# Performance work log

Hardware: AMD Instinct MI355X
Metric: run time of the kernel (lower is better)

## Reference

```python
import jax, jax.numpy as jnp
import numpy as np

# Dims: batch, seq, model dim, heads, routes-per-query, bleed-over alpha
B, S, D, H, K_ROUTES = 4, 512, 1024, 16, 64
HD = D // H                      # head_dim = 64
SCALE = 1.0 / float(np.sqrt(HD))
ALPHA = 0.25                     # neighbor bleed-over (forward arg default 0.0; >0 here)
CAUSAL = True
NEG = jnp.float32(-1e9)


def _build_routes(seq_len: int, k: int, depth: int = 8) -> np.ndarray:
    """Cantor-coordinate based positional routes (mirrors _build_positional_routes)."""
    pos = np.arange(seq_len, dtype=np.float64)
    x = pos / max(1, seq_len - 1)
    x = np.clip(x, 1e-6, 1.0 - 1e-6)
    val = np.zeros_like(x)
    factor = 0.5
    for _ in range(depth):
        xs = x * 3.0
        digit = xs.astype(np.int64)
        frac = xs - digit
        val = val + (digit == 2).astype(np.float64) * factor
        x = frac
        factor *= 0.5
    coords = np.clip(val, 0.0, 1.0)
    dist = np.abs(coords[:, None] - coords[None, :])            # [S,S]
    routes = np.argsort(dist, axis=1, kind='stable')[:, :k]     # k smallest distances
    return routes.astype(np.int32)


def setup_inputs() -> dict:
    key = jax.random.key(0)
    k0, k1, k2 = jax.random.split(key, 3)
    x = jax.random.normal(k0, (B, S, D), dtype=jnp.float32)
    # nn.Linear weights stored pre-transposed as [in, out] for clean matmul
    w_qkv = jax.random.normal(k1, (D, 3 * D), dtype=jnp.float32) * (1.0 / np.sqrt(D))
    b_qkv = jnp.zeros((3 * D,), dtype=jnp.float32)
    w_out = jax.random.normal(k2, (D, D), dtype=jnp.float32) * (1.0 / np.sqrt(D))
    b_out = jnp.zeros((D,), dtype=jnp.float32)
    routes = jnp.asarray(_build_routes(S, K_ROUTES), dtype=jnp.int32)  # [S, K]
    return {"x": x, "w_qkv": w_qkv, "b_qkv": b_qkv,
            "w_out": w_out, "b_out": b_out, "routes": routes}


def reference(x, w_qkv, b_qkv, w_out, b_out, routes):
    # QKV projection: [B,S,3D] -> [3,B,H,S,hd]
    qkv = (x @ w_qkv + b_qkv).reshape(B, S, 3, H, HD).transpose(2, 0, 3, 1, 4)
    q, k, v = qkv[0], qkv[1], qkv[2]                 # each [B,H,S,hd]

    r = routes                                        # [S,K]
    k_g = jnp.take(k, r, axis=2)                      # [B,H,S,K,hd]
    v_g = jnp.take(v, r, axis=2)
    if ALPHA > 0.0:
        rl = jnp.clip(r - 1, 0, S - 1)
        rr = jnp.clip(r + 1, 0, S - 1)
        k_g = (1.0 - ALPHA) * k_g + (ALPHA / 2.0) * (jnp.take(k, rl, axis=2) + jnp.take(k, rr, axis=2))
        v_g = (1.0 - ALPHA) * v_g + (ALPHA / 2.0) * (jnp.take(v, rl, axis=2) + jnp.take(v, rr, axis=2))

    scores = jnp.einsum('bhqd,bhqkd->bhqk', q, k_g) * SCALE   # [B,H,S,K]
    if CAUSAL:
        # route index > query position is masked (each query always routes to itself)
        mask = r > jnp.arange(S, dtype=r.dtype)[:, None]       # [S,K]
        scores = jnp.where(mask[None, None], NEG, scores)

    attn = jax.nn.softmax(scores, axis=-1)
    out = jnp.einsum('bhqk,bhqkd->bhqd', attn, v_g)            # [B,H,S,hd]
    out = out.transpose(0, 2, 1, 3).reshape(B, S, D)
    return out @ w_out + b_out
```

## Files before the change

### kernel.cpp

```cpp
#include <hip/hip_runtime.h>
#include <hip/hip_bf16.h>

#define BB 4
#define SS 512
#define DD 1024
#define HH 16
#define KR 64
#define HDIM 64
#define THREE_D 3072
#define M_ROWS 2048
#define SCALE_F 0.125f

typedef __attribute__((ext_vector_type(8))) short short8;
typedef __attribute__((ext_vector_type(4))) float floatx4;

union F8 { short8 s; unsigned int u[4]; unsigned short h[8]; };

__device__ inline unsigned short f2bf(float f){
    union{float f; unsigned int u;} c; c.f = f;
    unsigned int u = c.u;
    return (unsigned short)((u + 0x7fffu + ((u >> 16) & 1u)) >> 16);
}

#define GLOAD_LDS16(g, l)                                                     \
    __builtin_amdgcn_global_load_lds(                                         \
        (const __attribute__((address_space(1))) unsigned int*)(g),           \
        (__attribute__((address_space(3))) unsigned int*)(l), 16, 0, 0)

__global__ __launch_bounds__(256) void cvtA_kernel(const float* __restrict__ x,
                                                   unsigned short* __restrict__ out)
{
    int gid = blockIdx.x * 256 + threadIdx.x;
    int r  = gid & 127;
    int c  = (gid >> 7) & 3;
    int kt = (gid >> 9) & 31;
    int mt = gid >> 14;
    const float* src = x + ((size_t)(mt * 128 + r)) * 1024 + kt * 32 + c * 8;
    float4 a = *(const float4*)src;
    float4 b = *(const float4*)(src + 4);
    F8 o;
    o.h[0] = f2bf(a.x); o.h[1] = f2bf(a.y); o.h[2] = f2bf(a.z); o.h[3] = f2bf(a.w);
    o.h[4] = f2bf(b.x); o.h[5] = f2bf(b.y); o.h[6] = f2bf(b.z); o.h[7] = f2bf(b.w);
    *(uint4*)(out + (size_t)gid * 8) = *(uint4*)&o;
}

__global__ __launch_bounds__(256) void cvtB_kernel(const float* __restrict__ w,
                                                   unsigned short* __restrict__ out, int N)
{
    int gid = blockIdx.x * 256 + threadIdx.x;
    int r  = gid & 127;
    int c  = (gid >> 7) & 3;
    int kt = (gid >> 9) & 31;
    int nt = gid >> 14;
    int n = nt * 128 + r;
    int kbase = kt * 32 + c * 8;
    F8 o;
#pragma unroll
    for (int j = 0; j < 8; ++j)
        o.h[j] = f2bf(w[(size_t)(kbase + j) * N + n]);
    *(uint4*)(out + (size_t)gid * 8) = *(uint4*)&o;
}

template<int EPI>
__global__ __launch_bounds__(256) void gemm_mfma(
    const unsigned short* __restrict__ Asw,
    const unsigned short* __restrict__ Bsw,
    const float* __restrict__ bias,
    float* __restrict__ Cout,
    unsigned short* __restrict__ qb, float* __restrict__ k_ws, float* __restrict__ v_ws,
    int N)
{
    __shared__ __align__(16) unsigned short Alds[4096];
    __shared__ __align__(16) unsigned short Blds[4096];

    const int tid  = threadIdx.x;
    const int lane = tid & 63;
    const int wid  = tid >> 6;
    const int l15  = lane & 15;
    const int quad = lane >> 4;
    const int wm   = (wid >> 1) * 64;
    const int wn   = (wid & 1) * 64;

    const unsigned short* Ak = Asw + (size_t)blockIdx.y * 131072;
    const unsigned short* Bk = Bsw + (size_t)blockIdx.x * 131072;

    floatx4 acc[4][4];
#pragma unroll
    for (int i = 0; i < 4; ++i)
#pragma unroll
        for (int j = 0; j < 4; ++j) acc[i][j] = (floatx4){0.f, 0.f, 0.f, 0.f};

    for (int kt = 0; kt < 32; ++kt) {
        const unsigned short* ga = Ak + kt * 4096 + wid * 1024 + lane * 8;
        const unsigned short* gb = Bk + kt * 4096 + wid * 1024 + lane * 8;
        GLOAD_LDS16(ga,       Alds + wid * 1024);
        GLOAD_LDS16(ga + 512, Alds + wid * 1024 + 512);
        GLOAD_LDS16(gb,       Blds + wid * 1024);
        GLOAD_LDS16(gb + 512, Blds + wid * 1024 + 512);
        __syncthreads();

        F8 af[4], bf[4];
#pragma unroll
        for (int mi = 0; mi < 4; ++mi)
            af[mi] = *(const F8*)(Alds + (size_t)(quad * 128 + wm + mi * 16 + l15) * 8);
#pragma unroll
        for (int ni = 0; ni < 4; ++ni)
            bf[ni] = *(const F8*)(Blds + (size_t)(quad * 128 + wn + ni * 16 + l15) * 8);
#pragma unroll
        for (int mi = 0; mi < 4; ++mi)
#pragma unroll
            for (int ni = 0; ni < 4; ++ni)
                acc[mi][ni] = __builtin_amdgcn_mfma_f32_16x16x32_bf16(
                    af[mi].s, bf[ni].s, acc[mi][ni], 0, 0, 0);
        __syncthreads();
    }

    const int m0 = blockIdx.y * 128;
    const int n0 = blockIdx.x * 128;
#pragma unroll
    for (int mi = 0; mi < 4; ++mi) {
#pragma unroll
        for (int ni = 0; ni < 4; ++ni) {
            int col = n0 + wn + ni * 16 + l15;
            float bv = bias[col];
#pragma unroll
            for (int r = 0; r < 4; ++r) {
                int row = m0 + wm + mi * 16 + quad * 4 + r;
                float val = acc[mi][ni][r] + bv;
                if (EPI == 0) {
                    Cout[(size_t)row * N + col] = val;
                } else {
                    int which = col >> 10, rem = col & 1023;
                    int h = rem >> 6, hd = rem & 63;
                    int b = row >> 9, s = row & 511;
                    size_t off = (((size_t)(b * HH + h) * SS) + s) * HDIM + hd;
                    if (which == 0)      qb[off]   = f2bf(val);
                    else if (which == 1) k_ws[off] = val;
                    else                 v_ws[off] = val;
                }
            }
        }
    }
}

__global__ __launch_bounds__(256) void blend_tr_kernel(
    const float* __restrict__ k_ws, const float* __restrict__ v_ws,
    unsigned short* __restrict__ K2g, unsigned short* __restrict__ Vtg)
{
    __shared__ float kt[130][65];
    __shared__ float vt[130][65];
    const int bh = blockIdx.x >> 2;
    const int sb = (blockIdx.x & 3) * 128;
    const int tid = threadIdx.x;
    const float* kbase = k_ws + (size_t)bh * SS * HDIM;
    const float* vbase = v_ws + (size_t)bh * SS * HDIM;

    for (int i = tid; i < 130 * 16; i += 256) {
        int row = i >> 4, c4 = (i & 15) << 2;
        int s = sb + row - 1; s = s < 0 ? 0 : (s > SS - 1 ? SS - 1 : s);
        float4 kk = *(const float4*)(kbase + (size_t)s * 64 + c4);
        float4 vv = *(const float4*)(vbase + (size_t)s * 64 + c4);
        kt[row][c4] = kk.x; kt[row][c4+1] = kk.y; kt[row][c4+2] = kk.z; kt[row][c4+3] = kk.w;
        vt[row][c4] = vv.x; vt[row][c4+1] = vv.y; vt[row][c4+2] = vv.z; vt[row][c4+3] = vv.w;
    }
    __syncthreads();

    for (int i = tid; i < 128 * 16; i += 256) {
        int sl = i >> 4, c4 = (i & 15) << 2;
        ushort4 o;
        o.x = f2bf(0.75f * kt[sl+1][c4+0] + 0.125f * (kt[sl][c4+0] + kt[sl+2][c4+0]));
        o.y = f2bf(0.75f * kt[sl+1][c4+1] + 0.125f * (kt[sl][c4+1] + kt[sl+2][c4+1]));
        o.z = f2bf(0.75f * kt[sl+1][c4+2] + 0.125f * (kt[sl][c4+2] + kt[sl+2][c4+2]));
        o.w = f2bf(0.75f * kt[sl+1][c4+3] + 0.125f * (kt[sl][c4+3] + kt[sl+2][c4+3]));
        *(ushort4*)(K2g + ((size_t)bh * SS + sb + sl) * 64 + c4) = o;
    }
    for (int i = tid; i < 64 * 32; i += 256) {
        int d = i >> 5, s4 = (i & 31) << 2;
        ushort4 o;
        o.x = f2bf(0.75f * vt[s4+1][d] + 0.125f * (vt[s4+0][d] + vt[s4+2][d]));
        o.y = f2bf(0.75f * vt[s4+2][d] + 0.125f * (vt[s4+1][d] + vt[s4+3][d]));
        o.z = f2bf(0.75f * vt[s4+3][d] + 0.125f * (vt[s4+2][d] + vt[s4+4][d]));
        o.w = f2bf(0.75f * vt[s4+4][d] + 0.125f * (vt[s4+3][d] + vt[s4+5][d]));
        *(ushort4*)(Vtg + ((size_t)bh * 64 + d) * SS + sb + s4) = o;
    }
}

__global__ __launch_bounds__(256) void mask_kernel(const int* __restrict__ routes,
                                                   unsigned int* __restrict__ maskg)
{
    int q = blockIdx.x * 256 + threadIdx.x;
    unsigned int w[16];
#pragma unroll
    for (int i = 0; i < 16; ++i) w[i] = 0u;
    for (int j = 0; j < KR; ++j) {
        int r = routes[q * KR + j];
        if (r <= q) w[r >> 5] |= 1u << (r & 31);
    }
#pragma unroll
    for (int sw = 0; sw < 16; ++sw) maskg[sw * SS + q] = w[sw];
}

__global__ __launch_bounds__(512, 2) void attn_kernel(
    const unsigned short* __restrict__ qb,
    const unsigned short* __restrict__ K2g,
    const unsigned short* __restrict__ Vtg,
    const unsigned int* __restrict__ maskg,
    unsigned short* __restrict__ attn_sw)
{
    __shared__ __align__(16) unsigned short Ks[512 * 64];
    __shared__ __align__(16) unsigned short Vs[64 * 512];
    __shared__ __align__(16) unsigned short Ps[8 * 16 * 64];

    const int bh = blockIdx.x >> 2;
    const int qt = blockIdx.x & 3;
    const int b = bh >> 4, h = bh & 15;
    const int tid  = threadIdx.x;
    const int lane = tid & 63;
    const int wid  = tid >> 6;
    const int l15  = lane & 15;
    const int quad = lane >> 4;

    {
        const uint4* src = (const uint4*)(K2g + (size_t)bh * (SS * 64));
        uint4* dst = (uint4*)Ks;
        for (int c = tid; c < 4096; c += 512) {
            int s = c >> 3, cc = c & 7;
            dst[(s << 3) | (cc ^ (s & 7))] = src[c];
        }
        const uint4* srcv = (const uint4*)(Vtg + (size_t)bh * (64 * SS));
        uint4* dstv = (uint4*)Vs;
        for (int c = tid; c < 4096; c += 512) {
            int d = c >> 6, sc = c & 63;
            dstv[(d << 6) | (sc & 56) | ((sc ^ d) & 7)] = srcv[c];
        }
    }
    __syncthreads();

    const int qbase = qt * 128 + wid * 16;
    const int q = qbase + l15;

    F8 qf[2];
    {
        const unsigned short* qrow = qb + ((size_t)bh * SS + q) * 64;
        qf[0] = *(const F8*)(qrow + quad * 8);
        qf[1] = *(const F8*)(qrow + 32 + quad * 8);
    }

    floatx4 accS[32];
#pragma unroll
    for (int st = 0; st < 32; ++st) {
        int srow = st * 16 + l15;
        const F8 k0 = *(const F8*)(Ks + (((srow << 3) | ( quad      ^ (srow & 7))) << 3));
        const F8 k1 = *(const F8*)(Ks + (((srow << 3) | ((4 + quad) ^ (srow & 7))) << 3));
        floatx4 a = (floatx4){0.f, 0.f, 0.f, 0.f};
        a = __builtin_amdgcn_mfma_f32_16x16x32_bf16(k0.s, qf[0].s, a, 0, 0, 0);
        a = __builtin_amdgcn_mfma_f32_16x16x32_bf16(k1.s, qf[1].s, a, 0, 0, 0);
        accS[st] = a;
    }

    float m = -1e30f;
    unsigned int mw = 0;
#pragma unroll
    for (int st = 0; st < 32; ++st) {
        if ((st & 1) == 0) mw = maskg[(st >> 1) * SS + q];
        int sbase = (st & 1) * 16 + quad * 4;
        floatx4 a = accS[st];
#pragma unroll
        for (int r = 0; r < 4; ++r) {
            float v = ((mw >> (sbase + r)) & 1u) ? a[r] * SCALE_F : -1e30f;
            a[r] = v;
            m = fmaxf(m, v);
        }
        accS[st] = a;
    }
    m = fmaxf(m, __shfl_xor(m, 16));
    m = fmaxf(m, __shfl_xor(m, 32));

    floatx4 accO[4];
#pragma unroll
    for (int dt = 0; dt < 4; ++dt) accO[dt] = (floatx4){0.f, 0.f, 0.f, 0.f};
    float lsum = 0.f;
    unsigned int* Pw = (unsigned int*)Ps + wid * 512;

#pragma unroll
    for (int ch = 0; ch < 8; ++ch) {
#pragma unroll
        for (int t = 0; t < 4; ++t) {
            floatx4 a = accS[ch * 4 + t];
            float e0 = __expf(a[0] - m), e1 = __expf(a[1] - m);
            float e2 = __expf(a[2] - m), e3 = __expf(a[3] - m);
            lsum += (e0 + e1) + (e2 + e3);
            unsigned int w0 = (unsigned int)f2bf(e0) | ((unsigned int)f2bf(e1) << 16);
            unsigned int w1 = (unsigned int)f2bf(e2) | ((unsigned int)f2bf(e3) << 16);
            int off0 = t * 8 + quad * 2;
            int off1 = off0 + 1;
            Pw[l15 * 32 + ((((off0 >> 2) ^ (l15 & 7)) << 2) | (off0 & 3))] = w0;
            Pw[l15 * 32 + ((((off1 >> 2) ^ (l15 & 7)) << 2) | (off1 & 3))] = w1;
        }
        F8 pa[2];
#pragma unroll
        for (int ks = 0; ks < 2; ++ks) {
            int ci = ks * 4 + quad;
            pa[ks] = *(const F8*)((const unsigned short*)(Pw + l15 * 32) +
                                  ((ci ^ (l15 & 7)) << 3));
        }
#pragma unroll
        for (int dt = 0; dt < 4; ++dt) {
            int d = dt * 16 + l15;
#pragma unroll
            for (int ks = 0; ks < 2; ++ks) {
                int sc = ch * 8 + ks * 4 + quad;
                const F8 bv = *(const F8*)(Vs + (((d << 6) | (sc & 56) | ((sc ^ d) & 7)) << 3));
                accO[dt] = __builtin_amdgcn_mfma_f32_16x16x32_bf16(pa[ks].s, bv.s, accO[dt], 0, 0, 0);
            }
        }
    }

    lsum += __shfl_xor(lsum, 16);
    lsum += __shfl_xor(lsum, 32);
    float inv = 1.0f / lsum;

    unsigned short* Ow = Ps + wid * 1024;
#pragma unroll
    for (int r = 0; r < 4; ++r) {
        float invr = __shfl(inv, quad * 4 + r);
#pragma unroll
        for (int dt = 0; dt < 4; ++dt)
            Ow[(quad * 4 + r) * 64 + dt * 16 + l15] = f2bf(accO[dt][r] * invr);
    }
#pragma unroll
    for (int i = 0; i < 2; ++i) {
        int ch = i * 64 + lane;
        int qlocal = ch >> 3, j = ch & 7;
        int qq = qt * 128 + wid * 16 + qlocal;
        int mrow = b * SS + qq;
        int mt = mrow >> 7, rr = mrow & 127;
        int kt2 = h * 2 + (j >> 2), c = j & 3;
        size_t gid = (((size_t)(mt * 32 + kt2) * 4 + c) * 128 + rr);
        *(uint4*)(attn_sw + gid * 8) = *(const uint4*)(Ow + qlocal * 64 + j * 8);
    }
}

extern "C" void kernel_launch(void* const* d_in, const int* in_sizes, int n_in,
                              void* d_out, int out_size, void* d_ws, size_t ws_size,
                              hipStream_t stream)
{
    const float* x     = (const float*)d_in[0];
    const float* w_qkv = (const float*)d_in[1];
    const float* b_qkv = (const float*)d_in[2];
    const float* w_out = (const float*)d_in[3];
    const float* b_out = (const float*)d_in[4];
    const int* routes  = (const int*)d_in[5];

    char* w = (char*)d_ws;
    unsigned short* xb_sw  = (unsigned short*)(w);
    unsigned short* wb1_sw = (unsigned short*)(w + (4u  << 20));
    unsigned short* wb2_sw = (unsigned short*)(w + (10u << 20));
    unsigned short* qbuf   = (unsigned short*)(w + (12u << 20));
    float*          k_ws   = (float*)(w + (16u << 20));
    float*          v_ws   = (float*)(w + (24u << 20));
    unsigned short* K2g    = (unsigned short*)(w + (32u << 20));
    unsigned short* Vtg    = (unsigned short*)(w + (36u << 20));
    unsigned short* attnsw = (unsigned short*)(w + (40u << 20));
    unsigned int*   maskg  = (unsigned int*)(w + (44u << 20));

    cvtA_kernel<<<1024, 256, 0, stream>>>(x, xb_sw);
    cvtB_kernel<<<1536, 256, 0, stream>>>(w_qkv, wb1_sw, THREE_D);
    cvtB_kernel<<<512, 256, 0, stream>>>(w_out, wb2_sw, DD);
    mask_kernel<<<2, 256, 0, stream>>>(routes, maskg);

    gemm_mfma<1><<<dim3(THREE_D / 128, M_ROWS / 128), 256, 0, stream>>>(
        xb_sw, wb1_sw, b_qkv, nullptr, qbuf, k_ws, v_ws, THREE_D);

    blend_tr_kernel<<<256, 256, 0, stream>>>(k_ws, v_ws, K2g, Vtg);

    attn_kernel<<<256, 512, 0, stream>>>(qbuf, K2g, Vtg, maskg, attnsw);

    gemm_mfma<0><<<dim3(DD / 128, M_ROWS / 128), 256, 0, stream>>>(
        attnsw, wb2_sw, b_out, (float*)d_out, nullptr, nullptr, nullptr, DD);
}
```

Baseline: 171.9 us.

## Stage QKV epilogue through LDS as bf16 and retile output GEMM

The QKV GEMM epilogue now writes bias-added results as bf16 into shared memory, then emits coalesced 16-byte stores into head-major Q/K/V buffers. Previously it made scattered scalar stores and kept K/V in fp32. The blend kernel now reads the bf16 K/V, which halves its input traffic. The output projection GEMM uses 64-row tiles, doubling the block count from 128 to 256 to fill more compute units. K/V are rounded to bf16 before blending, a small precision change.

```diff
diff --git a/kernel.cpp b/kernel.cpp
--- a/kernel.cpp
+++ b/kernel.cpp
@@ -16,6 +16,7 @@
 
 union F8 { short8 s; unsigned int u[4]; unsigned short h[8]; };
 
+__device__ inline float bfu(unsigned short h){ union{unsigned int u; float f;} c; c.u = ((unsigned int)h) << 16; return c.f; }
 __device__ inline unsigned short f2bf(float f){
     union{float f; unsigned int u;} c; c.f = f;
     unsigned int u = c.u;
@@ -61,17 +62,16 @@
     *(uint4*)(out + (size_t)gid * 8) = *(uint4*)&o;
 }
 
-template<int EPI>
-__global__ __launch_bounds__(256) void gemm_mfma(
+__global__ __launch_bounds__(256) void gemm_qkv(
     const unsigned short* __restrict__ Asw,
     const unsigned short* __restrict__ Bsw,
     const float* __restrict__ bias,
-    float* __restrict__ Cout,
-    unsigned short* __restrict__ qb, float* __restrict__ k_ws, float* __restrict__ v_ws,
-    int N)
-{
-    __shared__ __align__(16) unsigned short Alds[4096];
-    __shared__ __align__(16) unsigned short Blds[4096];
+    unsigned short* __restrict__ qb, unsigned short* __restrict__ kb,
+    unsigned short* __restrict__ vb)
+{
+    __shared__ __align__(16) unsigned short Sh[128 * 136];
+    unsigned short* Alds = Sh;
+    unsigned short* Blds = Sh + 4096;
 
     const int tid  = threadIdx.x;
     const int lane = tid & 63;
@@ -117,34 +117,103 @@
 
     const int m0 = blockIdx.y * 128;
     const int n0 = blockIdx.x * 128;
+
 #pragma unroll
     for (int mi = 0; mi < 4; ++mi) {
 #pragma unroll
         for (int ni = 0; ni < 4; ++ni) {
+            int col = wn + ni * 16 + l15;
+            float bv = bias[n0 + col];
+#pragma unroll
+            for (int r = 0; r < 4; ++r) {
+                int row = wm + mi * 16 + quad * 4 + r;
+                Sh[row * 136 + col] = f2bf(acc[mi][ni][r] + bv);
+            }
+        }
+    }
+    __syncthreads();
+
+    for (int i = tid; i < 2048; i += 256) {
+        int rr = i >> 4, cc = i & 15;
+        int grow = m0 + rr, gcol = n0 + cc * 8;
+        int b = grow >> 9, s = grow & 511;
+        int which = gcol >> 10, rem = gcol & 1023;
+        int h = rem >> 6, hd = rem & 63;
+        unsigned short* dst = (which == 0) ? qb : (which == 1) ? kb : vb;
+        uint4 val = *(const uint4*)(Sh + rr * 136 + cc * 8);
+        *(uint4*)(dst + (((size_t)(b * HH + h) * SS) + s) * HDIM + hd) = val;
+    }
+}
+
+__global__ __launch_bounds__(256) void gemm_out(
+    const unsigned short* __restrict__ Asw,
+    const unsigned short* __restrict__ Bsw,
+    const float* __restrict__ bias,
+    float* __restrict__ Cout)
+{
+    __shared__ __align__(16) unsigned short Alds[2048];
+    __shared__ __align__(16) unsigned short Blds[4096];
+
+    const int tid  = threadIdx.x;
+    const int lane = tid & 63;
+    const int wid  = tid >> 6;
+    const int l15  = lane & 15;
+    const int quad = lane >> 4;
+    const int mt64 = blockIdx.y;
+    const int mt   = mt64 >> 1;
+    const int rh   = (mt64 & 1) * 64;
+    const int nt   = blockIdx.x;
+    const int wn   = wid * 32;
+
+    floatx4 acc[4][2];
+#pragma unroll
+    for (int i = 0; i < 4; ++i)
+#pragma unroll
+        for (int j = 0; j < 2; ++j) acc[i][j] = (floatx4){0.f, 0.f, 0.f, 0.f};
+
+    for (int kt = 0; kt < 32; ++kt) {
+        const unsigned short* ga = Asw + ((size_t)(mt * 32 + kt) * 4 + wid) * 1024 + (rh + lane) * 8;
+        const unsigned short* gb = Bsw + (size_t)(nt * 32 + kt) * 4096 + wid * 1024 + lane * 8;
+        GLOAD_LDS16(ga,       Alds + (wid * 64 + lane) * 8);
+        GLOAD_LDS16(gb,       Blds + wid * 1024 + lane * 8);
+        GLOAD_LDS16(gb + 512, Blds + wid * 1024 + 512 + lane * 8);
+        __syncthreads();
+
+        F8 af[4], bf[2];
+#pragma unroll
+        for (int mi = 0; mi < 4; ++mi)
+            af[mi] = *(const F8*)(Alds + (size_t)(quad * 64 + mi * 16 + l15) * 8);
+#pragma unroll
+        for (int ni = 0; ni < 2; ++ni)
+            bf[ni] = *(const F8*)(Blds + (size_t)(quad * 128 + wn + ni * 16 + l15) * 8);
+#pragma unroll
+        for (int mi = 0; mi < 4; ++mi)
+#pragma unroll
+            for (int ni = 0; ni < 2; ++ni)
+                acc[mi][ni] = __builtin_amdgcn_mfma_f32_16x16x32_bf16(
+                    af[mi].s, bf[ni].s, acc[mi][ni], 0, 0, 0);
+        __syncthreads();
+    }
+
+    const int m0 = mt64 * 64;
+    const int n0 = nt * 128;
+#pragma unroll
+    for (int mi = 0; mi < 4; ++mi) {
+#pragma unroll
+        for (int ni = 0; ni < 2; ++ni) {
             int col = n0 + wn + ni * 16 + l15;
             float bv = bias[col];
 #pragma unroll
             for (int r = 0; r < 4; ++r) {
-                int row = m0 + wm + mi * 16 + quad * 4 + r;
-                float val = acc[mi][ni][r] + bv;
-                if (EPI == 0) {
-                    Cout[(size_t)row * N + col] = val;
-                } else {
-                    int which = col >> 10, rem = col & 1023;
-                    int h = rem >> 6, hd = rem & 63;
-                    int b = row >> 9, s = row & 511;
-                    size_t off = (((size_t)(b * HH + h) * SS) + s) * HDIM + hd;
-                    if (which == 0)      qb[off]   = f2bf(val);
-                    else if (which == 1) k_ws[off] = val;
-                    else                 v_ws[off] = val;
-                }
+                int row = m0 + mi * 16 + quad * 4 + r;
+                Cout[(size_t)row * DD + col] = acc[mi][ni][r] + bv;
             }
         }
     }
 }
 
 __global__ __launch_bounds__(256) void blend_tr_kernel(
-    const float* __restrict__ k_ws, const float* __restrict__ v_ws,
+    const unsigned short* __restrict__ kb, const unsigned short* __restrict__ vb,
     unsigned short* __restrict__ K2g, unsigned short* __restrict__ Vtg)
 {
     __shared__ float kt[130][65];
@@ -152,16 +221,19 @@
     const int bh = blockIdx.x >> 2;
     const int sb = (blockIdx.x & 3) * 128;
     const int tid = threadIdx.x;
-    const float* kbase = k_ws + (size_t)bh * SS * HDIM;
-    const float* vbase = v_ws + (size_t)bh * SS * HDIM;
-
-    for (int i = tid; i < 130 * 16; i += 256) {
-        int row = i >> 4, c4 = (i & 15) << 2;
+    const unsigned short* kbase = kb + (size_t)bh * SS * HDIM;
+    const unsigned short* vbase = vb + (size_t)bh * SS * HDIM;
+
+    for (int i = tid; i < 130 * 8; i += 256) {
+        int row = i >> 3, c8 = (i & 7) << 3;
         int s = sb + row - 1; s = s < 0 ? 0 : (s > SS - 1 ? SS - 1 : s);
-        float4 kk = *(const float4*)(kbase + (size_t)s * 64 + c4);
-        float4 vv = *(const float4*)(vbase + (size_t)s * 64 + c4);
-        kt[row][c4] = kk.x; kt[row][c4+1] = kk.y; kt[row][c4+2] = kk.z; kt[row][c4+3] = kk.w;
-        vt[row][c4] = vv.x; vt[row][c4+1] = vv.y; vt[row][c4+2] = vv.z; vt[row][c4+3] = vv.w;
+        F8 kk = *(const F8*)(kbase + (size_t)s * 64 + c8);
+        F8 vv = *(const F8*)(vbase + (size_t)s * 64 + c8);
+#pragma unroll
+        for (int j = 0; j < 8; ++j) {
+            kt[row][c8 + j] = bfu(kk.h[j]);
+            vt[row][c8 + j] = bfu(vv.h[j]);
+        }
     }
     __syncthreads();
 
@@ -357,25 +429,25 @@
     unsigned short* wb1_sw = (unsigned short*)(w + (4u  << 20));
     unsigned short* wb2_sw = (unsigned short*)(w + (10u << 20));
     unsigned short* qbuf   = (unsigned short*)(w + (12u << 20));
-    float*          k_ws   = (float*)(w + (16u << 20));
-    float*          v_ws   = (float*)(w + (24u << 20));
-    unsigned short* K2g    = (unsigned short*)(w + (32u << 20));
-    unsigned short* Vtg    = (unsigned short*)(w + (36u << 20));
-    unsigned short* attnsw = (unsigned short*)(w + (40u << 20));
-    unsigned int*   maskg  = (unsigned int*)(w + (44u << 20));
+    unsigned short* kbuf   = (unsigned short*)(w + (16u << 20));
+    unsigned short* vbuf   = (unsigned short*)(w + (20u << 20));
+    unsigned short* K2g    = (unsigned short*)(w + (24u << 20));
+    unsigned short* Vtg    = (unsigned short*)(w + (28u << 20));
+    unsigned short* attnsw = (unsigned short*)(w + (32u << 20));
+    unsigned int*   maskg  = (unsigned int*)(w + (36u << 20));
 
     cvtA_kernel<<<1024, 256, 0, stream>>>(x, xb_sw);
     cvtB_kernel<<<1536, 256, 0, stream>>>(w_qkv, wb1_sw, THREE_D);
     cvtB_kernel<<<512, 256, 0, stream>>>(w_out, wb2_sw, DD);
     mask_kernel<<<2, 256, 0, stream>>>(routes, maskg);
 
-    gemm_mfma<1><<<dim3(THREE_D / 128, M_ROWS / 128), 256, 0, stream>>>(
-        xb_sw, wb1_sw, b_qkv, nullptr, qbuf, k_ws, v_ws, THREE_D);
-
-    blend_tr_kernel<<<256, 256, 0, stream>>>(k_ws, v_ws, K2g, Vtg);
+    gemm_qkv<<<dim3(THREE_D / 128, M_ROWS / 128), 256, 0, stream>>>(
+        xb_sw, wb1_sw, b_qkv, qbuf, kbuf, vbuf);
+
+    blend_tr_kernel<<<256, 256, 0, stream>>>(kbuf, vbuf, K2g, Vtg);
 
     attn_kernel<<<256, 512, 0, stream>>>(qbuf, K2g, Vtg, maskg, attnsw);
 
-    gemm_mfma<0><<<dim3(DD / 128, M_ROWS / 128), 256, 0, stream>>>(
-        attnsw, wb2_sw, b_out, (float*)d_out, nullptr, nullptr, nullptr, DD);
-}
+    gemm_out<<<dim3(DD / 128, M_ROWS / 64), 256, 0, stream>>>(
+        attnsw, wb2_sw, b_out, (float*)d_out);
+}
```

Result: faster. 163.4 us (-5.0%).
